# Kernel optimization log

Measured on AMD Instinct MI355X. Metric: run time of the kernel, lower is better.

## Reference

```python
import jax, jax.numpy as jnp
import numpy as np

N_NODES = 50000
N_EDGES = 800000
IN_DIM = 128
HEADS = 8
HEAD_DIM = 16


def setup_inputs() -> dict:
    key = jax.random.key(0)
    ks = jax.random.split(key, 9)
    s = 1.0 / np.sqrt(IN_DIM)
    return {
        "h": jax.random.normal(ks[0], (N_NODES, IN_DIM), dtype=jnp.float32),
        "src": jax.random.randint(ks[1], (N_EDGES,), 0, N_NODES, dtype=jnp.int32),
        "dst": jax.random.randint(ks[2], (N_EDGES,), 0, N_NODES, dtype=jnp.int32),
        "WQ": jax.random.normal(ks[3], (IN_DIM, HEADS * HEAD_DIM), dtype=jnp.float32) * s,
        "bQ": jnp.zeros((HEADS * HEAD_DIM,), dtype=jnp.float32),
        "WK": jax.random.normal(ks[4], (IN_DIM, HEADS * HEAD_DIM), dtype=jnp.float32) * s,
        "bK": jnp.zeros((HEADS * HEAD_DIM,), dtype=jnp.float32),
        "WV": jax.random.normal(ks[5], (IN_DIM, HEADS * HEAD_DIM), dtype=jnp.float32) * s,
        "bV": jnp.zeros((HEADS * HEAD_DIM,), dtype=jnp.float32),
    }


def reference(h, src, dst, WQ, bQ, WK, bK, WV, bV):
    N = h.shape[0]
    sqrt_d = jnp.float32(np.sqrt(HEAD_DIM))
    # node projections, viewed as [N, H, D]
    Q = (h @ WQ + bQ).reshape(N, HEADS, HEAD_DIM)
    K = (h @ WK + bK).reshape(N, HEADS, HEAD_DIM)
    V = (h @ WV + bV).reshape(N, HEADS, HEAD_DIM)
    # edge scores: (K_src . Q_dst) per head, scaled exp with clamp [-5, 5]
    score = jnp.sum(K[src] * Q[dst], axis=-1, keepdims=True)  # [E, H, 1]
    score = jnp.exp(jnp.clip(score / sqrt_d, -5.0, 5.0))
    # segment-softmax denominator z and weighted V sum wV, both scattered to dst
    z = jax.ops.segment_sum(score, dst, num_segments=N)            # [N, H, 1]
    wV = jax.ops.segment_sum(V[src] * score, dst, num_segments=N)  # [N, H, D]
    # possible_empty: divide only where z > 0 (wV is 0 there anyway)
    head_out = jnp.where(z > 0, wV / jnp.where(z > 0, z, 1.0), wV)
    return head_out
```

## Files before the change

kernel.cpp:

```cpp
#include <hip/hip_runtime.h>
#include <math.h>

#define DIM 128
#define N_HEADS 8
#define HD 16

typedef __attribute__((ext_vector_type(8))) short bf16x8;
typedef __attribute__((ext_vector_type(4))) float f32x4;

__device__ __forceinline__ unsigned bf16pack2(float a, float b) {
    unsigned ua = __builtin_bit_cast(unsigned, a);
    unsigned ub = __builtin_bit_cast(unsigned, b);
    ua = (ua + 0x7FFFu + ((ua >> 16) & 1u)) >> 16;
    ub = (ub + 0x7FFFu + ((ub >> 16) & 1u)) >> 16;
    return ua | (ub << 16);
}
__device__ __forceinline__ float bf16lo(unsigned p) {
    return __builtin_bit_cast(float, p << 16);
}
__device__ __forceinline__ float bf16hi(unsigned p) {
    return __builtin_bit_cast(float, p & 0xFFFF0000u);
}

__global__ __launch_bounds__(256)
void convert_hist_kernel(const float* __restrict__ WQ, const float* __restrict__ bQ,
                         const float* __restrict__ WK, const float* __restrict__ bK,
                         const float* __restrict__ WV, const float* __restrict__ bV,
                         unsigned short* __restrict__ WT, float* __restrict__ bias384,
                         const int* __restrict__ dst, int* __restrict__ offs,
                         int nConv, int E)
{
    if ((int)blockIdx.x < nConv) {
        int idx = blockIdx.x * 256 + threadIdx.x;
        int c = idx >> 7, k = idx & 127;
        const float* W; const float* b; int col = c & 127;
        if (c < 128)      { W = WQ; b = bQ; }
        else if (c < 256) { W = WK; b = bK; }
        else              { W = WV; b = bV; }
        float v = W[k * DIM + col];
        WT[(size_t)c * DIM + k] = (unsigned short)(bf16pack2(v, 0.0f) & 0xFFFFu);
        if (k == 0) bias384[c] = b[col];
    } else {
        int e = ((int)blockIdx.x - nConv) * 256 + threadIdx.x;
        if (e < E) atomicAdd(&offs[dst[e]], 1);
    }
}

__global__ __launch_bounds__(256)
void scan_blocks_kernel(int* __restrict__ offs, int* __restrict__ bsum, int N)
{
    __shared__ int sd[256];
    const int t = threadIdx.x;
    const int i = blockIdx.x * 256 + t;
    int v = (i < N) ? offs[i] : 0;
    sd[t] = v;
    __syncthreads();
    #pragma unroll
    for (int o = 1; o < 256; o <<= 1) {
        int x = (t >= o) ? sd[t - o] : 0;
        __syncthreads();
        sd[t] += x;
        __syncthreads();
    }
    int incl = sd[t];
    if (i < N) offs[i] = incl - v;
    if (t == 255) bsum[blockIdx.x] = incl;
}

__global__ __launch_bounds__(256)
void scan_fixup_kernel(int* __restrict__ offs, int* __restrict__ cursor,
                       const int* __restrict__ bsum, int nb, int N, int E)
{
    __shared__ int sd[256];
    const int t = threadIdx.x;
    sd[t] = (t < nb && t < (int)blockIdx.x) ? bsum[t] : 0;
    __syncthreads();
    #pragma unroll
    for (int o = 128; o > 0; o >>= 1) {
        if (t < o) sd[t] += sd[t + o];
        __syncthreads();
    }
    const int base = sd[0];
    int i = blockIdx.x * 256 + t;
    if (i < N) {
        int v = offs[i] + base;
        offs[i]   = v;
        cursor[i] = v;
    }
    if (i == 0) offs[N] = E;
}

__global__ __launch_bounds__(256)
void scatter_kernel(const int* __restrict__ src, const int* __restrict__ dst,
                    int* __restrict__ cursor, int* __restrict__ srcs, int E)
{
    int e = blockIdx.x * 256 + threadIdx.x;
    if (e < E) {
        int d   = dst[e];
        int pos = atomicAdd(&cursor[d], 1);
        srcs[pos] = src[e];
    }
}

__global__ __launch_bounds__(256)
void qkv_mfma_kernel(const float* __restrict__ h,
                     const unsigned short* __restrict__ WT,
                     const float* __restrict__ bias384,
                     float* __restrict__ Q, unsigned* __restrict__ KVd,
                     int N)
{
    __shared__ unsigned short hs[64 * 136];
    const int tid = threadIdx.x;
    const int n0  = blockIdx.x * 64;

    #pragma unroll
    for (int i = 0; i < 4; ++i) {
        int lin  = i * 256 + tid;
        int node = lin >> 4;
        int k0   = (lin & 15) * 8;
        int gn   = n0 + node;
        float4 a0, a1;
        if (gn < N) {
            a0 = *(const float4*)(h + (size_t)gn * DIM + k0);
            a1 = *(const float4*)(h + (size_t)gn * DIM + k0 + 4);
        } else {
            a0 = make_float4(0.f, 0.f, 0.f, 0.f);
            a1 = a0;
        }
        uint4 p = make_uint4(bf16pack2(a0.x, a0.y), bf16pack2(a0.z, a0.w),
                             bf16pack2(a1.x, a1.y), bf16pack2(a1.z, a1.w));
        *(uint4*)(hs + node * 136 + k0) = p;
    }
    __syncthreads();

    const int wave   = tid >> 6;
    const int l      = tid & 63;
    const int lane16 = l & 15;
    const int quad   = l >> 4;
    const int wc0    = wave * 96;

    f32x4 acc[6][4];
    #pragma unroll
    for (int ct = 0; ct < 6; ++ct) {
        float4 bv = *(const float4*)(bias384 + wc0 + ct * 16 + quad * 4);
        #pragma unroll
        for (int rt = 0; rt < 4; ++rt)
            acc[ct][rt] = (f32x4){bv.x, bv.y, bv.z, bv.w};
    }

    #pragma unroll
    for (int ks = 0; ks < 4; ++ks) {
        bf16x8 a[6], b[4];
        #pragma unroll
        for (int ct = 0; ct < 6; ++ct)
            a[ct] = *(const bf16x8*)(WT + (size_t)(wc0 + ct * 16 + lane16) * DIM
                                         + ks * 32 + quad * 8);
        #pragma unroll
        for (int rt = 0; rt < 4; ++rt)
            b[rt] = *(const bf16x8*)(hs + (rt * 16 + lane16) * 136 + ks * 32 + quad * 8);
        #pragma unroll
        for (int ct = 0; ct < 6; ++ct)
            #pragma unroll
            for (int rt = 0; rt < 4; ++rt)
                acc[ct][rt] = __builtin_amdgcn_mfma_f32_16x16x32_bf16(
                    a[ct], b[rt], acc[ct][rt], 0, 0, 0);
    }

    #pragma unroll
    for (int ct = 0; ct < 6; ++ct) {
        const int col = wc0 + ct * 16 + quad * 4;
        #pragma unroll
        for (int rt = 0; rt < 4; ++rt) {
            int gn = n0 + rt * 16 + lane16;
            if (gn >= N) continue;
            f32x4 v = acc[ct][rt];
            if (col < 128) {
                *(float4*)(Q + (size_t)gn * DIM + col) =
                    make_float4(v[0], v[1], v[2], v[3]);
            } else if (col < 256) {
                int c = col - 128;
                size_t base = (size_t)gn * 128 + ((c >> 3) * 8) + ((c & 4) >> 1);
                KVd[base]     = bf16pack2(v[0], v[1]);
                KVd[base + 1] = bf16pack2(v[2], v[3]);
            } else {
                int c = col - 256;
                size_t base = (size_t)gn * 128 + ((c >> 3) * 8) + 4 + ((c & 4) >> 1);
                KVd[base]     = bf16pack2(v[0], v[1]);
                KVd[base + 1] = bf16pack2(v[2], v[3]);
            }
        }
    }
}

__global__ __launch_bounds__(256)
void aggregate_kernel(const int* __restrict__ offs, const int* __restrict__ srcs,
                      const float* __restrict__ Q, const unsigned* __restrict__ KVd,
                      float* __restrict__ out, int N)
{
    const int node = blockIdx.x * 4 + (threadIdx.x >> 6);
    if (node >= N) return;
    const int l    = threadIdx.x & 63;
    const int slot = l >> 4;
    const int c    = l & 15;

    const float4 qa = *(const float4*)(Q + (size_t)node * DIM + c * 8);
    const float4 qb = *(const float4*)(Q + (size_t)node * DIM + c * 8 + 4);

    const int start = offs[node];
    const int end   = offs[node + 1];

    float acc[8] = {0.f, 0.f, 0.f, 0.f, 0.f, 0.f, 0.f, 0.f};
    float zs = 0.f;

    int e = start;
    for (; e + 8 <= end; e += 8) {
        int s0 = srcs[e + slot];
        int s1 = srcs[e + 4 + slot];
        const uint4* p0 = (const uint4*)(KVd + (size_t)s0 * 128 + c * 8);
        const uint4* p1 = (const uint4*)(KVd + (size_t)s1 * 128 + c * 8);
        uint4 K0 = p0[0], V0 = p0[1];
        uint4 K1 = p1[0], V1 = p1[1];

        float d0 = bf16lo(K0.x) * qa.x + bf16hi(K0.x) * qa.y
                 + bf16lo(K0.y) * qa.z + bf16hi(K0.y) * qa.w
                 + bf16lo(K0.z) * qb.x + bf16hi(K0.z) * qb.y
                 + bf16lo(K0.w) * qb.z + bf16hi(K0.w) * qb.w;
        float d1 = bf16lo(K1.x) * qa.x + bf16hi(K1.x) * qa.y
                 + bf16lo(K1.y) * qa.z + bf16hi(K1.y) * qa.w
                 + bf16lo(K1.z) * qb.x + bf16hi(K1.z) * qb.y
                 + bf16lo(K1.w) * qb.z + bf16hi(K1.w) * qb.w;
        d0 += __shfl_xor(d0, 1);
        d1 += __shfl_xor(d1, 1);
        d0 = fminf(fmaxf(d0 * 0.25f, -5.0f), 5.0f);
        d1 = fminf(fmaxf(d1 * 0.25f, -5.0f), 5.0f);
        float w0 = __expf(d0);
        float w1 = __expf(d1);
        zs += w0 + w1;
        acc[0] += w0 * bf16lo(V0.x); acc[1] += w0 * bf16hi(V0.x);
        acc[2] += w0 * bf16lo(V0.y); acc[3] += w0 * bf16hi(V0.y);
        acc[4] += w0 * bf16lo(V0.z); acc[5] += w0 * bf16hi(V0.z);
        acc[6] += w0 * bf16lo(V0.w); acc[7] += w0 * bf16hi(V0.w);
        acc[0] += w1 * bf16lo(V1.x); acc[1] += w1 * bf16hi(V1.x);
        acc[2] += w1 * bf16lo(V1.y); acc[3] += w1 * bf16hi(V1.y);
        acc[4] += w1 * bf16lo(V1.z); acc[5] += w1 * bf16hi(V1.z);
        acc[6] += w1 * bf16lo(V1.w); acc[7] += w1 * bf16hi(V1.w);
    }
    for (; e < end; e += 4) {
        int  eg    = e + slot;
        bool valid = eg < end;
        int  s0    = srcs[valid ? eg : (end - 1)];
        const uint4* p0 = (const uint4*)(KVd + (size_t)s0 * 128 + c * 8);
        uint4 K0 = p0[0], V0 = p0[1];

        float d0 = bf16lo(K0.x) * qa.x + bf16hi(K0.x) * qa.y
                 + bf16lo(K0.y) * qa.z + bf16hi(K0.y) * qa.w
                 + bf16lo(K0.z) * qb.x + bf16hi(K0.z) * qb.y
                 + bf16lo(K0.w) * qb.z + bf16hi(K0.w) * qb.w;
        d0 += __shfl_xor(d0, 1);
        d0 = fminf(fmaxf(d0 * 0.25f, -5.0f), 5.0f);
        float w0 = valid ? __expf(d0) : 0.0f;
        zs += w0;
        acc[0] += w0 * bf16lo(V0.x); acc[1] += w0 * bf16hi(V0.x);
        acc[2] += w0 * bf16lo(V0.y); acc[3] += w0 * bf16hi(V0.y);
        acc[4] += w0 * bf16lo(V0.z); acc[5] += w0 * bf16hi(V0.z);
        acc[6] += w0 * bf16lo(V0.w); acc[7] += w0 * bf16hi(V0.w);
    }

    #pragma unroll
    for (int j = 0; j < 8; ++j) {
        acc[j] += __shfl_xor(acc[j], 16);
        acc[j] += __shfl_xor(acc[j], 32);
    }
    zs += __shfl_xor(zs, 16);
    zs += __shfl_xor(zs, 32);

    if (slot == 0) {
        float inv = (zs > 0.0f) ? (1.0f / zs) : 0.0f;
        *(float4*)(out + (size_t)node * DIM + c * 8) =
            make_float4(acc[0] * inv, acc[1] * inv, acc[2] * inv, acc[3] * inv);
        *(float4*)(out + (size_t)node * DIM + c * 8 + 4) =
            make_float4(acc[4] * inv, acc[5] * inv, acc[6] * inv, acc[7] * inv);
    }
}

extern "C" void kernel_launch(void* const* d_in, const int* in_sizes, int n_in,
                              void* d_out, int out_size, void* d_ws, size_t ws_size,
                              hipStream_t stream) {
    const float* h   = (const float*)d_in[0];
    const int*   src = (const int*)  d_in[1];
    const int*   dst = (const int*)  d_in[2];
    const float* WQ  = (const float*)d_in[3];
    const float* bQ  = (const float*)d_in[4];
    const float* WK  = (const float*)d_in[5];
    const float* bK  = (const float*)d_in[6];
    const float* WV  = (const float*)d_in[7];
    const float* bV  = (const float*)d_in[8];
    float* out = (float*)d_out;

    const int N  = in_sizes[0] / DIM;
    const int E  = in_sizes[1];
    const int NB = (N + 255) / 256;
    const int EB = (E + 255) / 256;
    const int nConv = (384 * DIM) / 256;

    char* w = (char*)d_ws;
    float*          Q       = (float*)w;           w += (size_t)N * DIM * sizeof(float);
    unsigned*       KVd     = (unsigned*)w;        w += (size_t)N * 128 * sizeof(unsigned);
    unsigned short* WT      = (unsigned short*)w;  w += (size_t)384 * DIM * sizeof(unsigned short);
    float*          bias384 = (float*)w;           w += 384 * sizeof(float);
    int*            offs    = (int*)w;             w += (size_t)(N + 1) * sizeof(int);
    int*            cursor  = (int*)w;             w += (size_t)N * sizeof(int);
    int*            bsum    = (int*)w;             w += 256 * sizeof(int);
    int*            srcs    = (int*)w;

    hipMemsetAsync(offs, 0, (size_t)(N + 1) * sizeof(int), stream);

    convert_hist_kernel<<<nConv + EB, 256, 0, stream>>>(WQ, bQ, WK, bK, WV, bV,
                                                        WT, bias384, dst, offs,
                                                        nConv, E);
    scan_blocks_kernel<<<NB, 256, 0, stream>>>(offs, bsum, N);
    scan_fixup_kernel<<<NB, 256, 0, stream>>>(offs, cursor, bsum, NB, N, E);
    scatter_kernel<<<EB, 256, 0, stream>>>(src, dst, cursor, srcs, E);
    qkv_mfma_kernel<<<(N + 63) / 64, 256, 0, stream>>>(h, WT, bias384, Q, KVd, N);
    aggregate_kernel<<<(N + 3) / 4, 256, 0, stream>>>(offs, srcs, Q, KVd, out, N);
}
```

Baseline: 265.0 us.

## Replace two-pass scan with single-block scan, drop cursor array, store Q in bf16

Replaces the two-kernel block scan plus fixup with a single 1024-thread scan kernel that uses wave shuffles and carries a running total across chunks. The scatter then atomically increments the offsets array in place, so after scatter offs[i] holds the end of segment i and the aggregate kernel reads start and end from offs[node-1] and offs[node]. This removes the cursor array and one launch. Q is also stored as bf16, halving its write and read traffic. The costs are a serial single-block scan over 50k entries and reduced precision in Q.

```diff
diff --git a/kernel.cpp b/kernel.cpp
--- a/kernel.cpp
+++ b/kernel.cpp
@@ -46,58 +46,57 @@
     }
 }
 
-__global__ __launch_bounds__(256)
-void scan_blocks_kernel(int* __restrict__ offs, int* __restrict__ bsum, int N)
-{
-    __shared__ int sd[256];
-    const int t = threadIdx.x;
-    const int i = blockIdx.x * 256 + t;
-    int v = (i < N) ? offs[i] : 0;
-    sd[t] = v;
+__global__ __launch_bounds__(1024)
+void scan_kernel(int* __restrict__ offs, int N)
+{
+    __shared__ int ws[16];
+    __shared__ int wbase[16];
+    __shared__ int carry_s;
+    const int t    = threadIdx.x;
+    const int wave = t >> 6;
+    const int lane = t & 63;
+    if (t == 0) carry_s = 0;
     __syncthreads();
-    #pragma unroll
-    for (int o = 1; o < 256; o <<= 1) {
-        int x = (t >= o) ? sd[t - o] : 0;
+
+    for (int base = 0; base < N; base += 1024) {
+        int i = base + t;
+        int v = (i < N) ? offs[i] : 0;
+        int s = v;
+        #pragma unroll
+        for (int o = 1; o < 64; o <<= 1) {
+            int x = __shfl_up(s, o);
+            if (lane >= o) s += x;
+        }
+        if (lane == 63) ws[wave] = s;
         __syncthreads();
-        sd[t] += x;
+        if (wave == 0) {
+            int wv = (lane < 16) ? ws[lane] : 0;
+            int sw = wv;
+            #pragma unroll
+            for (int o = 1; o < 16; o <<= 1) {
+                int x = __shfl_up(sw, o);
+                if (lane >= o) sw += x;
+            }
+            if (lane < 16) wbase[lane] = sw - wv;
+            if (lane == 15) ws[0] = sw;
+        }
         __syncthreads();
-    }
-    int incl = sd[t];
-    if (i < N) offs[i] = incl - v;
-    if (t == 255) bsum[blockIdx.x] = incl;
-}
-
-__global__ __launch_bounds__(256)
-void scan_fixup_kernel(int* __restrict__ offs, int* __restrict__ cursor,
-                       const int* __restrict__ bsum, int nb, int N, int E)
-{
-    __shared__ int sd[256];
-    const int t = threadIdx.x;
-    sd[t] = (t < nb && t < (int)blockIdx.x) ? bsum[t] : 0;
-    __syncthreads();
-    #pragma unroll
-    for (int o = 128; o > 0; o >>= 1) {
-        if (t < o) sd[t] += sd[t + o];
+        int carry = carry_s;
+        if (i < N) offs[i] = s - v + wbase[wave] + carry;
         __syncthreads();
-    }
-    const int base = sd[0];
-    int i = blockIdx.x * 256 + t;
-    if (i < N) {
-        int v = offs[i] + base;
-        offs[i]   = v;
-        cursor[i] = v;
-    }
-    if (i == 0) offs[N] = E;
+        if (t == 0) carry_s = carry + ws[0];
+        __syncthreads();
+    }
 }
 
 __global__ __launch_bounds__(256)
 void scatter_kernel(const int* __restrict__ src, const int* __restrict__ dst,
-                    int* __restrict__ cursor, int* __restrict__ srcs, int E)
+                    int* __restrict__ offs, int* __restrict__ srcs, int E)
 {
     int e = blockIdx.x * 256 + threadIdx.x;
     if (e < E) {
         int d   = dst[e];
-        int pos = atomicAdd(&cursor[d], 1);
+        int pos = atomicAdd(&offs[d], 1);
         srcs[pos] = src[e];
     }
 }
@@ -106,7 +105,7 @@
 void qkv_mfma_kernel(const float* __restrict__ h,
                      const unsigned short* __restrict__ WT,
                      const float* __restrict__ bias384,
-                     float* __restrict__ Q, unsigned* __restrict__ KVd,
+                     unsigned* __restrict__ Qd, unsigned* __restrict__ KVd,
                      int N)
 {
     __shared__ unsigned short hs[64 * 136];
@@ -175,8 +174,9 @@
             if (gn >= N) continue;
             f32x4 v = acc[ct][rt];
             if (col < 128) {
-                *(float4*)(Q + (size_t)gn * DIM + col) =
-                    make_float4(v[0], v[1], v[2], v[3]);
+                size_t base = (size_t)gn * 64 + (col >> 1);
+                Qd[base]     = bf16pack2(v[0], v[1]);
+                Qd[base + 1] = bf16pack2(v[2], v[3]);
             } else if (col < 256) {
                 int c = col - 128;
                 size_t base = (size_t)gn * 128 + ((c >> 3) * 8) + ((c & 4) >> 1);
@@ -194,7 +194,7 @@
 
 __global__ __launch_bounds__(256)
 void aggregate_kernel(const int* __restrict__ offs, const int* __restrict__ srcs,
-                      const float* __restrict__ Q, const unsigned* __restrict__ KVd,
+                      const unsigned* __restrict__ Qd, const unsigned* __restrict__ KVd,
                       float* __restrict__ out, int N)
 {
     const int node = blockIdx.x * 4 + (threadIdx.x >> 6);
@@ -203,11 +203,14 @@
     const int slot = l >> 4;
     const int c    = l & 15;
 
-    const float4 qa = *(const float4*)(Q + (size_t)node * DIM + c * 8);
-    const float4 qb = *(const float4*)(Q + (size_t)node * DIM + c * 8 + 4);
-
-    const int start = offs[node];
-    const int end   = offs[node + 1];
+    const uint4 qd = *(const uint4*)(Qd + (size_t)node * 64 + c * 4);
+    const float q0 = bf16lo(qd.x), q1 = bf16hi(qd.x);
+    const float q2 = bf16lo(qd.y), q3 = bf16hi(qd.y);
+    const float q4 = bf16lo(qd.z), q5 = bf16hi(qd.z);
+    const float q6 = bf16lo(qd.w), q7 = bf16hi(qd.w);
+
+    const int start = node ? offs[node - 1] : 0;
+    const int end   = offs[node];
 
     float acc[8] = {0.f, 0.f, 0.f, 0.f, 0.f, 0.f, 0.f, 0.f};
     float zs = 0.f;
@@ -221,14 +224,14 @@
         uint4 K0 = p0[0], V0 = p0[1];
         uint4 K1 = p1[0], V1 = p1[1];
 
-        float d0 = bf16lo(K0.x) * qa.x + bf16hi(K0.x) * qa.y
-                 + bf16lo(K0.y) * qa.z + bf16hi(K0.y) * qa.w
-                 + bf16lo(K0.z) * qb.x + bf16hi(K0.z) * qb.y
-                 + bf16lo(K0.w) * qb.z + bf16hi(K0.w) * qb.w;
-        float d1 = bf16lo(K1.x) * qa.x + bf16hi(K1.x) * qa.y
-                 + bf16lo(K1.y) * qa.z + bf16hi(K1.y) * qa.w
-                 + bf16lo(K1.z) * qb.x + bf16hi(K1.z) * qb.y
-                 + bf16lo(K1.w) * qb.z + bf16hi(K1.w) * qb.w;
+        float d0 = bf16lo(K0.x) * q0 + bf16hi(K0.x) * q1
+                 + bf16lo(K0.y) * q2 + bf16hi(K0.y) * q3
+                 + bf16lo(K0.z) * q4 + bf16hi(K0.z) * q5
+                 + bf16lo(K0.w) * q6 + bf16hi(K0.w) * q7;
+        float d1 = bf16lo(K1.x) * q0 + bf16hi(K1.x) * q1
+                 + bf16lo(K1.y) * q2 + bf16hi(K1.y) * q3
+                 + bf16lo(K1.z) * q4 + bf16hi(K1.z) * q5
+                 + bf16lo(K1.w) * q6 + bf16hi(K1.w) * q7;
         d0 += __shfl_xor(d0, 1);
         d1 += __shfl_xor(d1, 1);
         d0 = fminf(fmaxf(d0 * 0.25f, -5.0f), 5.0f);
@@ -252,10 +255,10 @@
         const uint4* p0 = (const uint4*)(KVd + (size_t)s0 * 128 + c * 8);
         uint4 K0 = p0[0], V0 = p0[1];
 
-        float d0 = bf16lo(K0.x) * qa.x + bf16hi(K0.x) * qa.y
-                 + bf16lo(K0.y) * qa.z + bf16hi(K0.y) * qa.w
-                 + bf16lo(K0.z) * qb.x + bf16hi(K0.z) * qb.y
-                 + bf16lo(K0.w) * qb.z + bf16hi(K0.w) * qb.w;
+        float d0 = bf16lo(K0.x) * q0 + bf16hi(K0.x) * q1
+                 + bf16lo(K0.y) * q2 + bf16hi(K0.y) * q3
+                 + bf16lo(K0.z) * q4 + bf16hi(K0.z) * q5
+                 + bf16lo(K0.w) * q6 + bf16hi(K0.w) * q7;
         d0 += __shfl_xor(d0, 1);
         d0 = fminf(fmaxf(d0 * 0.25f, -5.0f), 5.0f);
         float w0 = valid ? __expf(d0) : 0.0f;
@@ -299,28 +302,24 @@
 
     const int N  = in_sizes[0] / DIM;
     const int E  = in_sizes[1];
-    const int NB = (N + 255) / 256;
     const int EB = (E + 255) / 256;
     const int nConv = (384 * DIM) / 256;
 
     char* w = (char*)d_ws;
-    float*          Q       = (float*)w;           w += (size_t)N * DIM * sizeof(float);
+    unsigned*       Qd      = (unsigned*)w;        w += (size_t)N * 64  * sizeof(unsigned);
     unsigned*       KVd     = (unsigned*)w;        w += (size_t)N * 128 * sizeof(unsigned);
     unsigned short* WT      = (unsigned short*)w;  w += (size_t)384 * DIM * sizeof(unsigned short);
     float*          bias384 = (float*)w;           w += 384 * sizeof(float);
-    int*            offs    = (int*)w;             w += (size_t)(N + 1) * sizeof(int);
-    int*            cursor  = (int*)w;             w += (size_t)N * sizeof(int);
-    int*            bsum    = (int*)w;             w += 256 * sizeof(int);
+    int*            offs    = (int*)w;             w += (size_t)N * sizeof(int);
     int*            srcs    = (int*)w;
 
-    hipMemsetAsync(offs, 0, (size_t)(N + 1) * sizeof(int), stream);
+    hipMemsetAsync(offs, 0, (size_t)N * sizeof(int), stream);
 
     convert_hist_kernel<<<nConv + EB, 256, 0, stream>>>(WQ, bQ, WK, bK, WV, bV,
                                                         WT, bias384, dst, offs,
                                                         nConv, E);
-    scan_blocks_kernel<<<NB, 256, 0, stream>>>(offs, bsum, N);
-    scan_fixup_kernel<<<NB, 256, 0, stream>>>(offs, cursor, bsum, NB, N, E);
-    scatter_kernel<<<EB, 256, 0, stream>>>(src, dst, cursor, srcs, E);
-    qkv_mfma_kernel<<<(N + 63) / 64, 256, 0, stream>>>(h, WT, bias384, Q, KVd, N);
-    aggregate_kernel<<<(N + 3) / 4, 256, 0, stream>>>(offs, srcs, Q, KVd, out, N);
-}
+    qkv_mfma_kernel<<<(N + 63) / 64, 256, 0, stream>>>(h, WT, bias384, Qd, KVd, N);
+    scan_kernel<<<1, 1024, 0, stream>>>(offs, N);
+    scatter_kernel<<<EB, 256, 0, stream>>>(src, dst, offs, srcs, E);
+    aggregate_kernel<<<(N + 3) / 4, 256, 0, stream>>>(offs, srcs, Qd, KVd, out, N);
+}
```

Result: slower. 294.1 us (+11.0%).

## Store Q in bf16, reuse offsets as scatter cursor, unroll edge loop by four

Applied to the files above, without the earlier changes.

Q is now written and read as packed bf16, which halves its memory traffic in the projection and aggregation kernels at some cost in precision. The separate cursor array is dropped: the scatter atomics advance offs in place, so afterwards offs[i] holds the end of segment i and the aggregator reads start from offs[i-1]. The aggregation loop is rewritten to issue four edge gathers per slot per iteration with validity masks, which raises memory-level parallelism and removes the separate tail loop.

```diff
diff --git a/kernel.cpp b/kernel.cpp
--- a/kernel.cpp
+++ b/kernel.cpp
@@ -68,8 +68,8 @@
 }
 
 __global__ __launch_bounds__(256)
-void scan_fixup_kernel(int* __restrict__ offs, int* __restrict__ cursor,
-                       const int* __restrict__ bsum, int nb, int N, int E)
+void scan_fixup_kernel(int* __restrict__ offs, const int* __restrict__ bsum,
+                       int nb, int N)
 {
     __shared__ int sd[256];
     const int t = threadIdx.x;
@@ -82,22 +82,17 @@
     }
     const int base = sd[0];
     int i = blockIdx.x * 256 + t;
-    if (i < N) {
-        int v = offs[i] + base;
-        offs[i]   = v;
-        cursor[i] = v;
-    }
-    if (i == 0) offs[N] = E;
+    if (i < N) offs[i] += base;
 }
 
 __global__ __launch_bounds__(256)
 void scatter_kernel(const int* __restrict__ src, const int* __restrict__ dst,
-                    int* __restrict__ cursor, int* __restrict__ srcs, int E)
+                    int* __restrict__ offs, int* __restrict__ srcs, int E)
 {
     int e = blockIdx.x * 256 + threadIdx.x;
     if (e < E) {
         int d   = dst[e];
-        int pos = atomicAdd(&cursor[d], 1);
+        int pos = atomicAdd(&offs[d], 1);
         srcs[pos] = src[e];
     }
 }
@@ -106,7 +101,7 @@
 void qkv_mfma_kernel(const float* __restrict__ h,
                      const unsigned short* __restrict__ WT,
                      const float* __restrict__ bias384,
-                     float* __restrict__ Q, unsigned* __restrict__ KVd,
+                     unsigned* __restrict__ Qd, unsigned* __restrict__ KVd,
                      int N)
 {
     __shared__ unsigned short hs[64 * 136];
@@ -175,8 +170,9 @@
             if (gn >= N) continue;
             f32x4 v = acc[ct][rt];
             if (col < 128) {
-                *(float4*)(Q + (size_t)gn * DIM + col) =
-                    make_float4(v[0], v[1], v[2], v[3]);
+                size_t base = (size_t)gn * 64 + (col >> 1);
+                Qd[base]     = bf16pack2(v[0], v[1]);
+                Qd[base + 1] = bf16pack2(v[2], v[3]);
             } else if (col < 256) {
                 int c = col - 128;
                 size_t base = (size_t)gn * 128 + ((c >> 3) * 8) + ((c & 4) >> 1);
@@ -194,7 +190,7 @@
 
 __global__ __launch_bounds__(256)
 void aggregate_kernel(const int* __restrict__ offs, const int* __restrict__ srcs,
-                      const float* __restrict__ Q, const unsigned* __restrict__ KVd,
+                      const unsigned* __restrict__ Qd, const unsigned* __restrict__ KVd,
                       float* __restrict__ out, int N)
 {
     const int node = blockIdx.x * 4 + (threadIdx.x >> 6);
@@ -203,67 +199,52 @@
     const int slot = l >> 4;
     const int c    = l & 15;
 
-    const float4 qa = *(const float4*)(Q + (size_t)node * DIM + c * 8);
-    const float4 qb = *(const float4*)(Q + (size_t)node * DIM + c * 8 + 4);
-
-    const int start = offs[node];
-    const int end   = offs[node + 1];
+    const uint4 qd = *(const uint4*)(Qd + (size_t)node * 64 + c * 4);
+    const float q0 = bf16lo(qd.x), q1 = bf16hi(qd.x);
+    const float q2 = bf16lo(qd.y), q3 = bf16hi(qd.y);
+    const float q4 = bf16lo(qd.z), q5 = bf16hi(qd.z);
+    const float q6 = bf16lo(qd.w), q7 = bf16hi(qd.w);
+
+    const int start = node ? offs[node - 1] : 0;
+    const int end   = offs[node];
 
     float acc[8] = {0.f, 0.f, 0.f, 0.f, 0.f, 0.f, 0.f, 0.f};
     float zs = 0.f;
 
-    int e = start;
-    for (; e + 8 <= end; e += 8) {
-        int s0 = srcs[e + slot];
-        int s1 = srcs[e + 4 + slot];
-        const uint4* p0 = (const uint4*)(KVd + (size_t)s0 * 128 + c * 8);
-        const uint4* p1 = (const uint4*)(KVd + (size_t)s1 * 128 + c * 8);
-        uint4 K0 = p0[0], V0 = p0[1];
-        uint4 K1 = p1[0], V1 = p1[1];
-
-        float d0 = bf16lo(K0.x) * qa.x + bf16hi(K0.x) * qa.y
-                 + bf16lo(K0.y) * qa.z + bf16hi(K0.y) * qa.w
-                 + bf16lo(K0.z) * qb.x + bf16hi(K0.z) * qb.y
-                 + bf16lo(K0.w) * qb.z + bf16hi(K0.w) * qb.w;
-        float d1 = bf16lo(K1.x) * qa.x + bf16hi(K1.x) * qa.y
-                 + bf16lo(K1.y) * qa.z + bf16hi(K1.y) * qa.w
-                 + bf16lo(K1.z) * qb.x + bf16hi(K1.z) * qb.y
-                 + bf16lo(K1.w) * qb.z + bf16hi(K1.w) * qb.w;
-        d0 += __shfl_xor(d0, 1);
-        d1 += __shfl_xor(d1, 1);
-        d0 = fminf(fmaxf(d0 * 0.25f, -5.0f), 5.0f);
-        d1 = fminf(fmaxf(d1 * 0.25f, -5.0f), 5.0f);
-        float w0 = __expf(d0);
-        float w1 = __expf(d1);
-        zs += w0 + w1;
-        acc[0] += w0 * bf16lo(V0.x); acc[1] += w0 * bf16hi(V0.x);
-        acc[2] += w0 * bf16lo(V0.y); acc[3] += w0 * bf16hi(V0.y);
-        acc[4] += w0 * bf16lo(V0.z); acc[5] += w0 * bf16hi(V0.z);
-        acc[6] += w0 * bf16lo(V0.w); acc[7] += w0 * bf16hi(V0.w);
-        acc[0] += w1 * bf16lo(V1.x); acc[1] += w1 * bf16hi(V1.x);
-        acc[2] += w1 * bf16lo(V1.y); acc[3] += w1 * bf16hi(V1.y);
-        acc[4] += w1 * bf16lo(V1.z); acc[5] += w1 * bf16hi(V1.z);
-        acc[6] += w1 * bf16lo(V1.w); acc[7] += w1 * bf16hi(V1.w);
-    }
-    for (; e < end; e += 4) {
-        int  eg    = e + slot;
-        bool valid = eg < end;
-        int  s0    = srcs[valid ? eg : (end - 1)];
-        const uint4* p0 = (const uint4*)(KVd + (size_t)s0 * 128 + c * 8);
-        uint4 K0 = p0[0], V0 = p0[1];
-
-        float d0 = bf16lo(K0.x) * qa.x + bf16hi(K0.x) * qa.y
-                 + bf16lo(K0.y) * qa.z + bf16hi(K0.y) * qa.w
-                 + bf16lo(K0.z) * qb.x + bf16hi(K0.z) * qb.y
-                 + bf16lo(K0.w) * qb.z + bf16hi(K0.w) * qb.w;
-        d0 += __shfl_xor(d0, 1);
-        d0 = fminf(fmaxf(d0 * 0.25f, -5.0f), 5.0f);
-        float w0 = valid ? __expf(d0) : 0.0f;
-        zs += w0;
-        acc[0] += w0 * bf16lo(V0.x); acc[1] += w0 * bf16hi(V0.x);
-        acc[2] += w0 * bf16lo(V0.y); acc[3] += w0 * bf16hi(V0.y);
-        acc[4] += w0 * bf16lo(V0.z); acc[5] += w0 * bf16hi(V0.z);
-        acc[6] += w0 * bf16lo(V0.w); acc[7] += w0 * bf16hi(V0.w);
+    for (int eg = start; eg < end; eg += 16) {
+        bool val[4];
+        const uint4* p[4];
+        #pragma unroll
+        for (int j = 0; j < 4; ++j) {
+            int ee = eg + j * 4 + slot;
+            val[j] = ee < end;
+            int s  = srcs[val[j] ? ee : (end - 1)];
+            p[j]   = (const uint4*)(KVd + (size_t)s * 128 + c * 8);
+        }
+        uint4 K[4], V[4];
+        #pragma unroll
+        for (int j = 0; j < 4; ++j) { K[j] = p[j][0]; V[j] = p[j][1]; }
+
+        float d[4];
+        #pragma unroll
+        for (int j = 0; j < 4; ++j)
+            d[j] = bf16lo(K[j].x) * q0 + bf16hi(K[j].x) * q1
+                 + bf16lo(K[j].y) * q2 + bf16hi(K[j].y) * q3
+                 + bf16lo(K[j].z) * q4 + bf16hi(K[j].z) * q5
+                 + bf16lo(K[j].w) * q6 + bf16hi(K[j].w) * q7;
+        #pragma unroll
+        for (int j = 0; j < 4; ++j) d[j] += __shfl_xor(d[j], 1);
+
+        #pragma unroll
+        for (int j = 0; j < 4; ++j) {
+            float pc = fminf(fmaxf(d[j] * 0.25f, -5.0f), 5.0f);
+            float w  = val[j] ? __expf(pc) : 0.0f;
+            zs += w;
+            acc[0] += w * bf16lo(V[j].x); acc[1] += w * bf16hi(V[j].x);
+            acc[2] += w * bf16lo(V[j].y); acc[3] += w * bf16hi(V[j].y);
+            acc[4] += w * bf16lo(V[j].z); acc[5] += w * bf16hi(V[j].z);
+            acc[6] += w * bf16lo(V[j].w); acc[7] += w * bf16hi(V[j].w);
+        }
     }
 
     #pragma unroll
@@ -304,23 +285,22 @@
     const int nConv = (384 * DIM) / 256;
 
     char* w = (char*)d_ws;
-    float*          Q       = (float*)w;           w += (size_t)N * DIM * sizeof(float);
+    unsigned*       Qd      = (unsigned*)w;        w += (size_t)N * 64  * sizeof(unsigned);
     unsigned*       KVd     = (unsigned*)w;        w += (size_t)N * 128 * sizeof(unsigned);
     unsigned short* WT      = (unsigned short*)w;  w += (size_t)384 * DIM * sizeof(unsigned short);
     float*          bias384 = (float*)w;           w += 384 * sizeof(float);
-    int*            offs    = (int*)w;             w += (size_t)(N + 1) * sizeof(int);
-    int*            cursor  = (int*)w;             w += (size_t)N * sizeof(int);
+    int*            offs    = (int*)w;             w += (size_t)N * sizeof(int);
     int*            bsum    = (int*)w;             w += 256 * sizeof(int);
     int*            srcs    = (int*)w;
 
-    hipMemsetAsync(offs, 0, (size_t)(N + 1) * sizeof(int), stream);
+    hipMemsetAsync(offs, 0, (size_t)N * sizeof(int), stream);
 
     convert_hist_kernel<<<nConv + EB, 256, 0, stream>>>(WQ, bQ, WK, bK, WV, bV,
                                                         WT, bias384, dst, offs,
                                                         nConv, E);
     scan_blocks_kernel<<<NB, 256, 0, stream>>>(offs, bsum, N);
-    scan_fixup_kernel<<<NB, 256, 0, stream>>>(offs, cursor, bsum, NB, N, E);
-    scatter_kernel<<<EB, 256, 0, stream>>>(src, dst, cursor, srcs, E);
-    qkv_mfma_kernel<<<(N + 63) / 64, 256, 0, stream>>>(h, WT, bias384, Q, KVd, N);
-    aggregate_kernel<<<(N + 3) / 4, 256, 0, stream>>>(offs, srcs, Q, KVd, out, N);
-}
+    scan_fixup_kernel<<<NB, 256, 0, stream>>>(offs, bsum, NB, N);
+    scatter_kernel<<<EB, 256, 0, stream>>>(src, dst, offs, srcs, E);
+    qkv_mfma_kernel<<<(N + 63) / 64, 256, 0, stream>>>(h, WT, bias384, Qd, KVd, N);
+    aggregate_kernel<<<(N + 3) / 4, 256, 0, stream>>>(offs, srcs, Qd, KVd, out, N);
+}
```

Result: faster. 258.1 us (-2.6%).
